# Kernel tuning notes

Hardware: AMD Instinct MI355X
Metric: run time of the kernel (lower is better)

## Reference

```python
import jax, jax.numpy as jnp
import numpy as np


def setup_inputs() -> dict:
    key = jax.random.key(0)
    k1, k2 = jax.random.split(key)
    B, N = 2048, 2048
    y_prime = jax.random.normal(k1, (B, N, 3), dtype=jnp.float32)
    y = jax.random.normal(k2, (B, N, 3), dtype=jnp.float32)
    return {"y_prime": y_prime, "y": y}


def reference(y_prime, y):
    """Batched SVD-superimposer (Kabsch) RMSD, averaged over the batch.

    Faithful to Biopython's SVDSuperimposer as used by RMSDLoss:
      set(reference=y, coords=y_prime); run(); get_rms().
    """
    n_atoms = y.shape[1]
    # Center both point clouds (av1/av2 in SVDSuperimposer)
    c = y_prime - jnp.mean(y_prime, axis=1, keepdims=True)  # coords, [B,N,3]
    r = y - jnp.mean(y, axis=1, keepdims=True)              # reference, [B,N,3]
    # a = coords^T @ reference  -> [B,3,3]
    a = jnp.einsum('bni,bnj->bij', c, r)
    u, s, vt = jnp.linalg.svd(a, full_matrices=False)
    # rot = (vt^T u^T)^T = u @ vt; fix improper rotation (reflection) via det sign
    det = jnp.linalg.det(jnp.einsum('bik,bkj->bij', u, vt))  # [B]
    sign = jnp.sign(det)
    ones = jnp.ones_like(sign)
    flip = jnp.stack([ones, ones, sign], axis=-1)            # [B,3]
    rot = jnp.einsum('bik,bk,bkj->bij', u, flip, vt)         # [B,3,3]
    # transformed = centered_coords @ rot; compare to centered reference
    diff = jnp.einsum('bni,bij->bnj', c, rot) - r
    rms = jnp.sqrt(jnp.sum(diff * diff, axis=(1, 2)) / n_atoms)  # [B]
    return jnp.mean(rms)
```

## Files before the change

### kernel.cpp

```cpp
#include <hip/hip_runtime.h>
#include <cmath>


constexpr int BLOCK = 256;
constexpr int NWAVE = BLOCK / 64;
constexpr int NS = 17;

template<int N>
__global__ __launch_bounds__(BLOCK) void rmsd_kernel(
    const float* __restrict__ yp,
    const float* __restrict__ yr,
    float* __restrict__ rms_out)
{
    static_assert(N == BLOCK * 8, "one thread = 8 atoms = 6 float4");
    const int b   = blockIdx.x;
    const int tid = threadIdx.x;
    const size_t row = (size_t)b * (size_t)N * 3u;
    const float4* p4 = (const float4*)(yp + row) + tid * 6;
    const float4* q4 = (const float4*)(yr + row) + tid * 6;

    const float4 P0=p4[0], P1=p4[1], P2=p4[2], P3=p4[3], P4=p4[4], P5=p4[5];
    const float4 Q0=q4[0], Q1=q4[1], Q2=q4[2], Q3=q4[3], Q4=q4[4], Q5=q4[5];
    __builtin_amdgcn_sched_barrier(0);

    float s1x=0.f,s1y=0.f,s1z=0.f, s2x=0.f,s2y=0.f,s2z=0.f, sq1=0.f,sq2=0.f;
    float c00=0.f,c01=0.f,c02=0.f,c10=0.f,c11=0.f,c12=0.f,c20=0.f,c21=0.f,c22=0.f;

    auto accum4 = [&](const float4&a0,const float4&a1,const float4&a2,
                      const float4&b0,const float4&b1,const float4&b2){
        float px[4]={a0.x,a0.w,a1.z,a2.y};
        float py[4]={a0.y,a1.x,a1.w,a2.z};
        float pz[4]={a0.z,a1.y,a2.x,a2.w};
        float qx[4]={b0.x,b0.w,b1.z,b2.y};
        float qy[4]={b0.y,b1.x,b1.w,b2.z};
        float qz[4]={b0.z,b1.y,b2.x,b2.w};
        #pragma unroll
        for (int k=0;k<4;k++){
            s1x+=px[k]; s1y+=py[k]; s1z+=pz[k];
            s2x+=qx[k]; s2y+=qy[k]; s2z+=qz[k];
            sq1 = fmaf(px[k],px[k], fmaf(py[k],py[k], fmaf(pz[k],pz[k], sq1)));
            sq2 = fmaf(qx[k],qx[k], fmaf(qy[k],qy[k], fmaf(qz[k],qz[k], sq2)));
            c00=fmaf(px[k],qx[k],c00); c01=fmaf(px[k],qy[k],c01); c02=fmaf(px[k],qz[k],c02);
            c10=fmaf(py[k],qx[k],c10); c11=fmaf(py[k],qy[k],c11); c12=fmaf(py[k],qz[k],c12);
            c20=fmaf(pz[k],qx[k],c20); c21=fmaf(pz[k],qy[k],c21); c22=fmaf(pz[k],qz[k],c22);
        }
    };
    accum4(P0,P1,P2, Q0,Q1,Q2);
    accum4(P3,P4,P5, Q3,Q4,Q5);

    float vals[NS] = {s1x,s1y,s1z,s2x,s2y,s2z,sq1,sq2,
                      c00,c01,c02,c10,c11,c12,c20,c21,c22};
    __shared__ float sred[NWAVE][NS];
    const int wave = tid >> 6, lane = tid & 63;
    #pragma unroll
    for (int i = 0; i < NS; ++i) {
        float v = vals[i];
        #pragma unroll
        for (int off = 32; off > 0; off >>= 1) v += __shfl_down(v, off, 64);
        if (lane == 0) sred[wave][i] = v;
    }
    __syncthreads();

    if (tid == 0) {
        float t[NS];
        #pragma unroll
        for (int i = 0; i < NS; ++i) {
            float s = 0.f;
            #pragma unroll
            for (int w = 0; w < NWAVE; ++w) s += sred[w][i];
            t[i] = s;
        }
        const float fn = (float)N;
        const float m1x=t[0]/fn, m1y=t[1]/fn, m1z=t[2]/fn;
        const float m2x=t[3]/fn, m2y=t[4]/fn, m2z=t[5]/fn;
        const float E0 = (t[6] - fn*(m1x*m1x+m1y*m1y+m1z*m1z))
                       + (t[7] - fn*(m2x*m2x+m2y*m2y+m2z*m2z));
        const float A00=t[8] -fn*m1x*m2x, A01=t[9] -fn*m1x*m2y, A02=t[10]-fn*m1x*m2z;
        const float A10=t[11]-fn*m1y*m2x, A11=t[12]-fn*m1y*m2y, A12=t[13]-fn*m1y*m2z;
        const float A20=t[14]-fn*m1z*m2x, A21=t[15]-fn*m1z*m2y, A22=t[16]-fn*m1z*m2z;

        const float det = A00*(A11*A22-A12*A21)
                        - A01*(A10*A22-A12*A20)
                        + A02*(A10*A21-A11*A20);

        const float G00 = A00*A00+A10*A10+A20*A20;
        const float G01 = A00*A01+A10*A11+A20*A21;
        const float G02 = A00*A02+A10*A12+A20*A22;
        const float G11 = A01*A01+A11*A11+A21*A21;
        const float G12 = A01*A02+A11*A12+A21*A22;
        const float G22 = A02*A02+A12*A12+A22*A22;

        const float q  = (G00+G11+G22)*(1.f/3.f);
        const float p1 = G01*G01 + G02*G02 + G12*G12;
        const float p2 = (G00-q)*(G00-q)+(G11-q)*(G11-q)+(G22-q)*(G22-q) + 2.f*p1;
        const float p  = sqrtf(p2*(1.f/6.f));
        float e1, e2, e3;
        if (p < 1e-20f) {
            e1 = e2 = e3 = q;
        } else {
            const float ip = 1.f/p;
            const float C00=(G00-q)*ip, C01=G01*ip, C02=G02*ip;
            const float C11=(G11-q)*ip, C12=G12*ip, C22=(G22-q)*ip;
            float detC = C00*(C11*C22-C12*C12)
                       - C01*(C01*C22-C12*C02)
                       + C02*(C01*C12-C11*C02);
            float rr = fminf(1.f, fmaxf(-1.f, 0.5f*detC));
            const float phi = acosf(rr)*(1.f/3.f);
            e1 = q + 2.f*p*cosf(phi);
            e3 = q + 2.f*p*cosf(phi + 2.0943951023931953f);
            e2 = 3.f*q - e1 - e3;
        }
        const float sv0 = sqrtf(fmaxf(e1,0.f));
        const float sv1 = sqrtf(fmaxf(e2,0.f));
        const float sv2 = sqrtf(fmaxf(e3,0.f));
        const float trs = sv0 + sv1 + ((det >= 0.f) ? sv2 : -sv2);
        const float msd = fmaxf(0.f, (E0 - 2.f*trs)/fn);
        rms_out[b] = sqrtf(msd);
    }
}

__global__ __launch_bounds__(BLOCK) void mean_kernel(
    const float* __restrict__ rms, float* __restrict__ out, int B)
{
    const int tid = threadIdx.x;
    const float4* r4 = (const float4*)rms;
    float s = 0.f;
    for (int i = tid; i < B/4; i += BLOCK) {
        float4 v = r4[i];
        s += (v.x + v.y) + (v.z + v.w);
    }
    #pragma unroll
    for (int off = 32; off > 0; off >>= 1) s += __shfl_down(s, off, 64);
    __shared__ float sred[NWAVE];
    const int wave = tid >> 6, lane = tid & 63;
    if (lane == 0) sred[wave] = s;
    __syncthreads();
    if (tid == 0) {
        float tot = 0.f;
        #pragma unroll
        for (int w = 0; w < NWAVE; ++w) tot += sred[w];
        out[0] = tot / (float)B;
    }
}

extern "C" void kernel_launch(void* const* d_in, const int* in_sizes, int n_in,
                              void* d_out, int out_size, void* d_ws, size_t ws_size,
                              hipStream_t stream) {
    const float* yp = (const float*)d_in[0];
    const float* yr = (const float*)d_in[1];
    const int N = 2048;
    const int B = in_sizes[0] / (N * 3);
    float* rms_ws = (float*)d_ws;

    rmsd_kernel<2048><<<B, BLOCK, 0, stream>>>(yp, yr, rms_ws);
    mean_kernel<<<1, BLOCK, 0, stream>>>(rms_ws, (float*)d_out, B);
}
```

Baseline: 26.63 us.

## Process two batch rows per block with software-pipelined loads

Each block now handles two consecutive batch rows, and the grid is halved. Loads for the second row are issued before the first row's accumulation and reduction finish, so memory latency overlaps with compute and the serial solve. A min-blocks-per-CU hint of 4 is added to launch bounds. The trade-off is fewer blocks (1024) spread over the CUs, more live registers, and an extra __syncthreads per row.

```diff
diff --git a/kernel.cpp b/kernel.cpp
--- a/kernel.cpp
+++ b/kernel.cpp
@@ -7,21 +7,19 @@
 constexpr int NS = 17;
 
 template<int N>
-__global__ __launch_bounds__(BLOCK) void rmsd_kernel(
+__global__ __launch_bounds__(BLOCK, 4) void rmsd_kernel(
     const float* __restrict__ yp,
     const float* __restrict__ yr,
     float* __restrict__ rms_out)
 {
-    static_assert(N == BLOCK * 8, "one thread = 8 atoms = 6 float4");
+    static_assert(N == BLOCK * 8, "one thread = 8 atoms/row = 6 float4/row");
     const int b   = blockIdx.x;
     const int tid = threadIdx.x;
-    const size_t row = (size_t)b * (size_t)N * 3u;
-    const float4* p4 = (const float4*)(yp + row) + tid * 6;
-    const float4* q4 = (const float4*)(yr + row) + tid * 6;
+    const int wave = tid >> 6, lane = tid & 63;
+    constexpr int ROWF4 = N * 3 / 4;
 
-    const float4 P0=p4[0], P1=p4[1], P2=p4[2], P3=p4[3], P4=p4[4], P5=p4[5];
-    const float4 Q0=q4[0], Q1=q4[1], Q2=q4[2], Q3=q4[3], Q4=q4[4], Q5=q4[5];
-    __builtin_amdgcn_sched_barrier(0);
+    const float4* p0 = (const float4*)(yp + (size_t)(2*b) * N * 3) + tid * 6;
+    const float4* q0 = (const float4*)(yr + (size_t)(2*b) * N * 3) + tid * 6;
 
     float s1x=0.f,s1y=0.f,s1z=0.f, s2x=0.f,s2y=0.f,s2z=0.f, sq1=0.f,sq2=0.f;
     float c00=0.f,c01=0.f,c02=0.f,c10=0.f,c11=0.f,c12=0.f,c20=0.f,c21=0.f,c22=0.f;
@@ -45,78 +43,112 @@
             c20=fmaf(pz[k],qx[k],c20); c21=fmaf(pz[k],qy[k],c21); c22=fmaf(pz[k],qz[k],c22);
         }
     };
-    accum4(P0,P1,P2, Q0,Q1,Q2);
-    accum4(P3,P4,P5, Q3,Q4,Q5);
 
-    float vals[NS] = {s1x,s1y,s1z,s2x,s2y,s2z,sq1,sq2,
-                      c00,c01,c02,c10,c11,c12,c20,c21,c22};
     __shared__ float sred[NWAVE][NS];
-    const int wave = tid >> 6, lane = tid & 63;
-    #pragma unroll
-    for (int i = 0; i < NS; ++i) {
-        float v = vals[i];
-        #pragma unroll
-        for (int off = 32; off > 0; off >>= 1) v += __shfl_down(v, off, 64);
-        if (lane == 0) sred[wave][i] = v;
-    }
-    __syncthreads();
 
-    if (tid == 0) {
-        float t[NS];
+    auto reduce_solve = [&](int row){
+        float vals[NS] = {s1x,s1y,s1z,s2x,s2y,s2z,sq1,sq2,
+                          c00,c01,c02,c10,c11,c12,c20,c21,c22};
         #pragma unroll
         for (int i = 0; i < NS; ++i) {
-            float s = 0.f;
+            float v = vals[i];
             #pragma unroll
-            for (int w = 0; w < NWAVE; ++w) s += sred[w][i];
-            t[i] = s;
+            for (int off = 32; off > 0; off >>= 1) v += __shfl_down(v, off, 64);
+            vals[i] = v;
         }
-        const float fn = (float)N;
-        const float m1x=t[0]/fn, m1y=t[1]/fn, m1z=t[2]/fn;
-        const float m2x=t[3]/fn, m2y=t[4]/fn, m2z=t[5]/fn;
-        const float E0 = (t[6] - fn*(m1x*m1x+m1y*m1y+m1z*m1z))
-                       + (t[7] - fn*(m2x*m2x+m2y*m2y+m2z*m2z));
-        const float A00=t[8] -fn*m1x*m2x, A01=t[9] -fn*m1x*m2y, A02=t[10]-fn*m1x*m2z;
-        const float A10=t[11]-fn*m1y*m2x, A11=t[12]-fn*m1y*m2y, A12=t[13]-fn*m1y*m2z;
-        const float A20=t[14]-fn*m1z*m2x, A21=t[15]-fn*m1z*m2y, A22=t[16]-fn*m1z*m2z;
+        __syncthreads();
+        if (lane == 0) {
+            #pragma unroll
+            for (int i = 0; i < NS; ++i) sred[wave][i] = vals[i];
+        }
+        __syncthreads();
+        if (tid == 0) {
+            float t[NS];
+            #pragma unroll
+            for (int i = 0; i < NS; ++i) {
+                float s = 0.f;
+                #pragma unroll
+                for (int w = 0; w < NWAVE; ++w) s += sred[w][i];
+                t[i] = s;
+            }
+            const float fn = (float)N;
+            const float m1x=t[0]/fn, m1y=t[1]/fn, m1z=t[2]/fn;
+            const float m2x=t[3]/fn, m2y=t[4]/fn, m2z=t[5]/fn;
+            const float E0 = (t[6] - fn*(m1x*m1x+m1y*m1y+m1z*m1z))
+                           + (t[7] - fn*(m2x*m2x+m2y*m2y+m2z*m2z));
+            const float A00=t[8] -fn*m1x*m2x, A01=t[9] -fn*m1x*m2y, A02=t[10]-fn*m1x*m2z;
+            const float A10=t[11]-fn*m1y*m2x, A11=t[12]-fn*m1y*m2y, A12=t[13]-fn*m1y*m2z;
+            const float A20=t[14]-fn*m1z*m2x, A21=t[15]-fn*m1z*m2y, A22=t[16]-fn*m1z*m2z;
 
-        const float det = A00*(A11*A22-A12*A21)
-                        - A01*(A10*A22-A12*A20)
-                        + A02*(A10*A21-A11*A20);
+            const float det = A00*(A11*A22-A12*A21)
+                            - A01*(A10*A22-A12*A20)
+                            + A02*(A10*A21-A11*A20);
 
-        const float G00 = A00*A00+A10*A10+A20*A20;
-        const float G01 = A00*A01+A10*A11+A20*A21;
-        const float G02 = A00*A02+A10*A12+A20*A22;
-        const float G11 = A01*A01+A11*A11+A21*A21;
-        const float G12 = A01*A02+A11*A12+A21*A22;
-        const float G22 = A02*A02+A12*A12+A22*A22;
+            const float G00 = A00*A00+A10*A10+A20*A20;
+            const float G01 = A00*A01+A10*A11+A20*A21;
+            const float G02 = A00*A02+A10*A12+A20*A22;
+            const float G11 = A01*A01+A11*A11+A21*A21;
+            const float G12 = A01*A02+A11*A12+A21*A22;
+            const float G22 = A02*A02+A12*A12+A22*A22;
 
-        const float q  = (G00+G11+G22)*(1.f/3.f);
-        const float p1 = G01*G01 + G02*G02 + G12*G12;
-        const float p2 = (G00-q)*(G00-q)+(G11-q)*(G11-q)+(G22-q)*(G22-q) + 2.f*p1;
-        const float p  = sqrtf(p2*(1.f/6.f));
-        float e1, e2, e3;
-        if (p < 1e-20f) {
-            e1 = e2 = e3 = q;
-        } else {
-            const float ip = 1.f/p;
-            const float C00=(G00-q)*ip, C01=G01*ip, C02=G02*ip;
-            const float C11=(G11-q)*ip, C12=G12*ip, C22=(G22-q)*ip;
-            float detC = C00*(C11*C22-C12*C12)
-                       - C01*(C01*C22-C12*C02)
-                       + C02*(C01*C12-C11*C02);
-            float rr = fminf(1.f, fmaxf(-1.f, 0.5f*detC));
-            const float phi = acosf(rr)*(1.f/3.f);
-            e1 = q + 2.f*p*cosf(phi);
-            e3 = q + 2.f*p*cosf(phi + 2.0943951023931953f);
-            e2 = 3.f*q - e1 - e3;
+            const float q  = (G00+G11+G22)*(1.f/3.f);
+            const float p1 = G01*G01 + G02*G02 + G12*G12;
+            const float p2 = (G00-q)*(G00-q)+(G11-q)*(G11-q)+(G22-q)*(G22-q) + 2.f*p1;
+            const float p  = sqrtf(p2*(1.f/6.f));
+            float e1, e2, e3;
+            if (p < 1e-20f) {
+                e1 = e2 = e3 = q;
+            } else {
+                const float ip = 1.f/p;
+                const float C00=(G00-q)*ip, C01=G01*ip, C02=G02*ip;
+                const float C11=(G11-q)*ip, C12=G12*ip, C22=(G22-q)*ip;
+                float detC = C00*(C11*C22-C12*C12)
+                           - C01*(C01*C22-C12*C02)
+                           + C02*(C01*C12-C11*C02);
+                float rr = fminf(1.f, fmaxf(-1.f, 0.5f*detC));
+                const float phi = acosf(rr)*(1.f/3.f);
+                e1 = q + 2.f*p*cosf(phi);
+                e3 = q + 2.f*p*cosf(phi + 2.0943951023931953f);
+                e2 = 3.f*q - e1 - e3;
+            }
+            const float sv0 = sqrtf(fmaxf(e1,0.f));
+            const float sv1 = sqrtf(fmaxf(e2,0.f));
+            const float sv2 = sqrtf(fmaxf(e3,0.f));
+            const float trs = sv0 + sv1 + ((det >= 0.f) ? sv2 : -sv2);
+            const float msd = fmaxf(0.f, (E0 - 2.f*trs)/fn);
+            rms_out[row] = sqrtf(msd);
         }
-        const float sv0 = sqrtf(fmaxf(e1,0.f));
-        const float sv1 = sqrtf(fmaxf(e2,0.f));
-        const float sv2 = sqrtf(fmaxf(e3,0.f));
-        const float trs = sv0 + sv1 + ((det >= 0.f) ? sv2 : -sv2);
-        const float msd = fmaxf(0.f, (E0 - 2.f*trs)/fn);
-        rms_out[b] = sqrtf(msd);
-    }
+        s1x=s1y=s1z=s2x=s2y=s2z=sq1=sq2=0.f;
+        c00=c01=c02=c10=c11=c12=c20=c21=c22=0.f;
+    };
+
+    float4 Pa0=p0[0], Pa1=p0[1], Pa2=p0[2];
+    float4 Qa0=q0[0], Qa1=q0[1], Qa2=q0[2];
+    float4 Pb0=p0[3], Pb1=p0[4], Pb2=p0[5];
+    float4 Qb0=q0[3], Qb1=q0[4], Qb2=q0[5];
+    __builtin_amdgcn_sched_barrier(0);
+
+    accum4(Pa0,Pa1,Pa2, Qa0,Qa1,Qa2);
+    __builtin_amdgcn_sched_barrier(0);
+
+    Pa0=p0[ROWF4+0]; Pa1=p0[ROWF4+1]; Pa2=p0[ROWF4+2];
+    Qa0=q0[ROWF4+0]; Qa1=q0[ROWF4+1]; Qa2=q0[ROWF4+2];
+    __builtin_amdgcn_sched_barrier(0);
+
+    accum4(Pb0,Pb1,Pb2, Qb0,Qb1,Qb2);
+    __builtin_amdgcn_sched_barrier(0);
+
+    reduce_solve(2*b);
+
+    Pb0=p0[ROWF4+3]; Pb1=p0[ROWF4+4]; Pb2=p0[ROWF4+5];
+    Qb0=q0[ROWF4+3]; Qb1=q0[ROWF4+4]; Qb2=q0[ROWF4+5];
+    __builtin_amdgcn_sched_barrier(0);
+
+    accum4(Pa0,Pa1,Pa2, Qa0,Qa1,Qa2);
+    __builtin_amdgcn_sched_barrier(0);
+    accum4(Pb0,Pb1,Pb2, Qb0,Qb1,Qb2);
+
+    reduce_solve(2*b + 1);
 }
 
 __global__ __launch_bounds__(BLOCK) void mean_kernel(
@@ -152,6 +184,6 @@
     const int B = in_sizes[0] / (N * 3);
     float* rms_ws = (float*)d_ws;
 
-    rmsd_kernel<2048><<<B, BLOCK, 0, stream>>>(yp, yr, rms_ws);
+    rmsd_kernel<2048><<<B/2, BLOCK, 0, stream>>>(yp, yr, rms_ws);
     mean_kernel<<<1, BLOCK, 0, stream>>>(rms_ws, (float*)d_out, B);
 }
```

Result: slower. 30.76 us (+15.5%).
